# Kernel optimization log

Measured on AMD Instinct MI355X. Metric: run time of the kernel, lower is better.

Reference implementation:

```python
import jax, jax.numpy as jnp
import numpy as np

HID, H, KV, D = 2048, 16, 4, 128
B, L = 8, 1024
T = B * L
EPS = 1e-6
NEG = -1e9


def _rms(x, w):
    # RMSNorm over head_dim in fp32
    var = jnp.mean(x.astype(jnp.float32) ** 2, axis=-1, keepdims=True)
    return (x.astype(jnp.float32) * jax.lax.rsqrt(var + EPS)).astype(x.dtype) * w


def _rot_half(x):
    x1, x2 = jnp.split(x, 2, axis=-1)
    return jnp.concatenate([-x2, x1], axis=-1)


def setup_inputs() -> dict:
    key = jax.random.key(0)
    ks = jax.random.split(key, 24)
    inp = {}
    inp['packed_sequence'] = jax.random.normal(ks[0], (T, HID), jnp.float32) * 0.02
    # RoPE tables: positions restart per sample
    pos = jnp.tile(jnp.arange(L, dtype=jnp.float32), B)  # [T]
    inv_freq = 1.0 / (10000.0 ** (jnp.arange(0, D, 2, dtype=jnp.float32) / D))
    ang = pos[:, None] * inv_freq[None, :]  # [T, D/2]
    inp['cos'] = jnp.concatenate([jnp.cos(ang), jnp.cos(ang)], axis=-1)
    inp['sin'] = jnp.concatenate([jnp.sin(ang), jnp.sin(ang)], axis=-1)
    # per-sample causal additive mask [B, L, L]
    causal = jnp.tril(jnp.ones((L, L), bool))
    inp['attn_bias'] = jnp.broadcast_to(jnp.where(causal, 0.0, NEG).astype(jnp.float32), (B, L, L))
    inp['gen_mask'] = jax.random.randint(ks[1], (T,), 0, 2, jnp.int32)
    s = 0.02
    inp['Wq'] = jax.random.normal(ks[2], (H * D, HID), jnp.float32) * s
    inp['bq'] = jnp.zeros((H * D,), jnp.float32)
    inp['Wqg'] = jax.random.normal(ks[3], (H * D, HID), jnp.float32) * s
    inp['bqg'] = jnp.zeros((H * D,), jnp.float32)
    inp['Wk'] = jax.random.normal(ks[4], (KV * D, HID), jnp.float32) * s
    inp['bk'] = jnp.zeros((KV * D,), jnp.float32)
    inp['Wkg'] = jax.random.normal(ks[5], (KV * D, HID), jnp.float32) * s
    inp['bkg'] = jnp.zeros((KV * D,), jnp.float32)
    inp['Wv'] = jax.random.normal(ks[6], (KV * D, HID), jnp.float32) * s
    inp['bv'] = jnp.zeros((KV * D,), jnp.float32)
    inp['Wvg'] = jax.random.normal(ks[7], (KV * D, HID), jnp.float32) * s
    inp['bvg'] = jnp.zeros((KV * D,), jnp.float32)
    inp['Wo'] = jax.random.normal(ks[8], (HID, H * D), jnp.float32) * s
    inp['Wog'] = jax.random.normal(ks[9], (HID, H * D), jnp.float32) * s
    inp['q_norm_w'] = jnp.ones((D,), jnp.float32)
    inp['q_norm_gen_w'] = jnp.ones((D,), jnp.float32)
    inp['k_norm_w'] = jnp.ones((D,), jnp.float32)
    inp['k_norm_gen_w'] = jnp.ones((D,), jnp.float32)
    return inp


def reference(packed_sequence, cos, sin, attn_bias, gen_mask,
              Wq, bq, Wqg, bqg, Wk, bk, Wkg, bkg, Wv, bv, Wvg, bvg,
              Wo, Wog, q_norm_w, q_norm_gen_w, k_norm_w, k_norm_gen_w):
    route = (gen_mask > 0)[:, None]  # [T,1]; und/gen indexes partition tokens -> select
    # dual-path QKV projections (scatter into zero buffers == per-token select)
    q = jnp.where(route, packed_sequence @ Wqg.T + bqg, packed_sequence @ Wq.T + bq)
    k = jnp.where(route, packed_sequence @ Wkg.T + bkg, packed_sequence @ Wk.T + bk)
    v = jnp.where(route, packed_sequence @ Wvg.T + bvg, packed_sequence @ Wv.T + bv)
    q = q.reshape(T, H, D)
    k = k.reshape(T, KV, D)
    v = v.reshape(T, KV, D)
    rh = route[:, :, None]  # [T,1,1]
    # dual-path per-head-dim RMSNorm
    q = jnp.where(rh, _rms(q, q_norm_gen_w), _rms(q, q_norm_w))
    k = jnp.where(rh, _rms(k, k_norm_gen_w), _rms(k, k_norm_w))
    # RoPE (broadcast over heads, unsqueeze_dim=1)
    c, s = cos[:, None, :], sin[:, None, :]
    q = q * c + _rot_half(q) * s
    k = k * c + _rot_half(k) * s
    # GQA: repeat kv heads to H
    k = jnp.repeat(k, H // KV, axis=1)
    v = jnp.repeat(v, H // KV, axis=1)
    # ragged attention, equal sample lens -> batched SDPA with per-sample masks
    qb = q.reshape(B, L, H, D)
    kb = k.reshape(B, L, H, D)
    vb = v.reshape(B, L, H, D)
    scores = jnp.einsum('blhd,bmhd->bhlm', qb, kb) / np.sqrt(D).astype(np.float32)
    scores = scores + attn_bias[:, None, :, :]
    p = jax.nn.softmax(scores, axis=-1)
    o = jnp.einsum('bhlm,bmhd->blhd', p, vb).reshape(T, H * D)
    # dual-path output projection (no bias)
    return jnp.where(route, o @ Wog.T, o @ Wo.T)
```

## Files before the change

kernel.cpp:

```cpp
#include <hip/hip_runtime.h>

#define T_TOK 8192
#define HID   2048
#define NH    16
#define NKV   4
#define HD    128

typedef __attribute__((ext_vector_type(8))) short short8;
typedef __attribute__((ext_vector_type(4))) float f32x4;
typedef __attribute__((ext_vector_type(4))) unsigned short us4;

__device__ __forceinline__ unsigned short f2b(float f) {
  union { float f; unsigned int u; } x; x.f = f;
  unsigned int u = x.u;
  return (unsigned short)((u + 0x7FFFu + ((u >> 16) & 1u)) >> 16);
}
__device__ __forceinline__ float b2f(unsigned short u) {
  union { float f; unsigned int u; } x; x.u = ((unsigned int)u) << 16; return x.f;
}

__device__ __forceinline__ void ld_lds16(const unsigned short* g, unsigned short* l) {
  __builtin_amdgcn_global_load_lds(
      (const __attribute__((address_space(1))) unsigned int*)g,
      (__attribute__((address_space(3))) unsigned int*)l, 16, 0, 0);
}

__device__ __forceinline__ int xcd_swz(int orig, int nwg) {
  int q = nwg >> 3;
  return (orig & 7) * q + (orig >> 3);
}

__global__ __launch_bounds__(1024) void scan_route(const int* __restrict__ gm,
                                                   int* __restrict__ perm,
                                                   int* __restrict__ n0p) {
  __shared__ int cnt[1024];
  int tid = threadIdx.x;
  int base = tid * 8;
  int r[8]; int c0 = 0;
#pragma unroll
  for (int i = 0; i < 8; i++) { r[i] = gm[base + i] > 0 ? 1 : 0; c0 += 1 - r[i]; }
  cnt[tid] = c0;
  __syncthreads();
  for (int off = 1; off < 1024; off <<= 1) {
    int add = (tid >= off) ? cnt[tid - off] : 0;
    __syncthreads();
    cnt[tid] += add;
    __syncthreads();
  }
  int incl = cnt[tid];
  int total0 = cnt[1023];
  int p0 = incl - c0;
  int p1 = total0 + (base - (incl - c0));
#pragma unroll
  for (int i = 0; i < 8; i++) {
    int t = base + i;
    if (r[i] == 0) perm[p0++] = t;
    else           perm[p1++] = t;
  }
  if (tid == 0) n0p[0] = total0;
}

struct ConvArgs {
  const float* src[9];
  unsigned short* dst[9];
  int blk_end[9];
};

__global__ __launch_bounds__(256) void convert_all(ConvArgs a) {
  int blk = blockIdx.x;
  int s = 0;
  while (blk >= a.blk_end[s]) s++;
  int local = blk - (s ? a.blk_end[s - 1] : 0);
  int i = local * 1024 + threadIdx.x * 4;
  float4 v = *(const float4*)(a.src[s] + i);
  us4 o = { f2b(v.x), f2b(v.y), f2b(v.z), f2b(v.w) };
  *(us4*)(a.dst[s] + i) = o;
}

#define BM  128
#define BK  64

__device__ __forceinline__ void gemm_core(
    const unsigned short* __restrict__ Xb,
    const unsigned short* __restrict__ W,
    const float* __restrict__ bias,
    const int* __restrict__ perm,
    int r0, int r1, int col0, int N,
    float* __restrict__ outF, unsigned short* __restrict__ outB,
    unsigned short* As, unsigned short* Bs)
{
  int tid = threadIdx.x;
  int lane = tid & 63, wid = tid >> 6;
  int quad = lane >> 4, l15 = lane & 15;
  int wr = (wid >> 1) * 64, wc = (wid & 1) * 64;
  int lrow = lane >> 3;
  int sc8 = (lane & 7) ^ (lrow & 7);

  const unsigned short* ag[4]; const unsigned short* bg[4];
  unsigned short* al[4]; unsigned short* bl[4];
#pragma unroll
  for (int i = 0; i < 4; i++) {
    int row = wid * 32 + i * 8 + lrow;
    int gr = r0 + row; if (gr > r1 - 1) gr = r1 - 1;
    ag[i] = Xb + (size_t)perm[gr] * HID + sc8 * 8;
    bg[i] = W + (size_t)(col0 + row) * HID + sc8 * 8;
    al[i] = As + (wid * 32 + i * 8) * BK;
    bl[i] = Bs + (wid * 32 + i * 8) * BK;
  }

  f32x4 zero = {0.f, 0.f, 0.f, 0.f};
  f32x4 acc[4][4];
#pragma unroll
  for (int a = 0; a < 4; a++)
#pragma unroll
    for (int b = 0; b < 4; b++) acc[a][b] = zero;

  for (int k0 = 0; k0 < HID; k0 += BK) {
#pragma unroll
    for (int i = 0; i < 4; i++) {
      ld_lds16(ag[i] + k0, al[i]);
      ld_lds16(bg[i] + k0, bl[i]);
    }
    __syncthreads();
#pragma unroll
    for (int kk = 0; kk < 2; kk++) {
      int cswz = ((kk * 4 + quad) ^ (l15 & 7)) * 8;
      short8 af[4], bf[4];
#pragma unroll
      for (int mt = 0; mt < 4; mt++)
        af[mt] = *(const short8*)&As[(wr + mt * 16 + l15) * BK + cswz];
#pragma unroll
      for (int nt = 0; nt < 4; nt++)
        bf[nt] = *(const short8*)&Bs[(wc + nt * 16 + l15) * BK + cswz];
#pragma unroll
      for (int mt = 0; mt < 4; mt++)
#pragma unroll
        for (int nt = 0; nt < 4; nt++)
          acc[mt][nt] = __builtin_amdgcn_mfma_f32_16x16x32_bf16(af[mt], bf[nt], acc[mt][nt], 0, 0, 0);
    }
    __syncthreads();
  }

#pragma unroll
  for (int mt = 0; mt < 4; mt++) {
#pragma unroll
    for (int r = 0; r < 4; r++) {
      int lr = wr + mt * 16 + quad * 4 + r;
      int gr = r0 + lr;
      if (gr >= r1) continue;
      int tok = perm[gr];
#pragma unroll
      for (int nt = 0; nt < 4; nt++) {
        int col = col0 + wc + nt * 16 + l15;
        float v = acc[mt][nt][r];
        if (bias) v += bias[col];
        if (outF) outF[(size_t)tok * N + col] = v;
        else      outB[(size_t)tok * N + col] = f2b(v);
      }
    }
  }
}

#define QKV_GX 64
#define QKV_GY 24
__global__ __launch_bounds__(256, 3) void gemm_qkv(
    const unsigned short* __restrict__ xb,
    const unsigned short* wq0, const unsigned short* wq1,
    const float* bq0, const float* bq1,
    const unsigned short* wk0, const unsigned short* wk1,
    const float* bk0, const float* bk1,
    const unsigned short* wv0, const unsigned short* wv1,
    const float* bv0, const float* bv1,
    unsigned short* qraw, unsigned short* kraw, unsigned short* vb,
    const int* __restrict__ perm, const int* __restrict__ n0p)
{
  __shared__ unsigned short As[BM * BK];
  __shared__ unsigned short Bs[BM * BK];
  int orig = blockIdx.x + QKV_GX * (blockIdx.y + QKV_GY * blockIdx.z);
  int wg = xcd_swz(orig, QKV_GX * QKV_GY * 2);
  int bx = wg % QKV_GX, by = (wg / QKV_GX) % QKV_GY, set = wg / (QKV_GX * QKV_GY);

  int n0 = n0p[0];
  int r0, r1;
  if (set == 0) { r0 = bx * BM; if (r0 >= n0) return; r1 = (r0 + BM < n0) ? r0 + BM : n0; }
  else          { r0 = n0 + bx * BM; if (r0 >= T_TOK) return; r1 = (r0 + BM < T_TOK) ? r0 + BM : T_TOK; }
  const unsigned short* w; const float* bias;
  unsigned short* ob; int col0, N;
  if (by < 16)      { w = set ? wq1 : wq0; bias = set ? bq1 : bq0; col0 = by * 128;        N = HID; ob = qraw; }
  else if (by < 20) { w = set ? wk1 : wk0; bias = set ? bk1 : bk0; col0 = (by - 16) * 128; N = 512; ob = kraw; }
  else              { w = set ? wv1 : wv0; bias = set ? bv1 : bv0; col0 = (by - 20) * 128; N = 512; ob = vb; }
  gemm_core(xb, w, bias, perm, r0, r1, col0, N, nullptr, ob, As, Bs);
}

#define OUT_GX 64
#define OUT_GY 16
__global__ __launch_bounds__(256, 3) void gemm_out(
    const unsigned short* __restrict__ obuf,
    const unsigned short* wo0, const unsigned short* wo1,
    float* __restrict__ out,
    const int* __restrict__ perm, const int* __restrict__ n0p)
{
  __shared__ unsigned short As[BM * BK];
  __shared__ unsigned short Bs[BM * BK];
  int orig = blockIdx.x + OUT_GX * (blockIdx.y + OUT_GY * blockIdx.z);
  int wg = xcd_swz(orig, OUT_GX * OUT_GY * 2);
  int bx = wg % OUT_GX, by = (wg / OUT_GX) % OUT_GY, set = wg / (OUT_GX * OUT_GY);

  int n0 = n0p[0];
  int r0, r1;
  if (set == 0) { r0 = bx * BM; if (r0 >= n0) return; r1 = (r0 + BM < n0) ? r0 + BM : n0; }
  else          { r0 = n0 + bx * BM; if (r0 >= T_TOK) return; r1 = (r0 + BM < T_TOK) ? r0 + BM : T_TOK; }
  gemm_core(obuf, set ? wo1 : wo0, nullptr, perm, r0, r1, by * 128, HID, out, nullptr, As, Bs);
}

__global__ __launch_bounds__(256) void rms_rope_all(
    const unsigned short* __restrict__ qin, unsigned short* __restrict__ qout,
    const unsigned short* __restrict__ kin, unsigned short* __restrict__ kout,
    const float* __restrict__ cosb, const float* __restrict__ sinb,
    const int* __restrict__ gm,
    const float* __restrict__ qwn, const float* __restrict__ qwg,
    const float* __restrict__ kwn, const float* __restrict__ kwg)
{
  int wvid = blockIdx.x * 4 + (threadIdx.x >> 6);
  int lane = threadIdx.x & 63;
  const unsigned short* in; unsigned short* outp;
  const float* wn; const float* wg; int t, h, nh;
  if (wvid < T_TOK * NH) {
    in = qin; outp = qout; wn = qwn; wg = qwg; t = wvid >> 4; h = wvid & 15; nh = NH;
  } else {
    int w2 = wvid - T_TOK * NH;
    in = kin; outp = kout; wn = kwn; wg = kwg; t = w2 >> 2; h = w2 & 3; nh = NKV;
  }
  size_t off = ((size_t)t * nh + h) * HD;
  float x1 = b2f(in[off + lane]), x2 = b2f(in[off + 64 + lane]);
  float ss = x1 * x1 + x2 * x2;
#pragma unroll
  for (int o = 32; o > 0; o >>= 1) ss += __shfl_xor(ss, o, 64);
  float inv = rsqrtf(ss * (1.0f / 128.0f) + 1e-6f);
  const float* w = (gm[t] > 0) ? wg : wn;
  float n1 = x1 * inv * w[lane];
  float n2 = x2 * inv * w[lane + 64];
  float c1 = cosb[t * HD + lane],      s1 = sinb[t * HD + lane];
  float c2 = cosb[t * HD + 64 + lane], s2 = sinb[t * HD + 64 + lane];
  outp[off + lane]      = f2b(n1 * c1 - n2 * s1);
  outp[off + 64 + lane] = f2b(n2 * c2 + n1 * s2);
}

__global__ __launch_bounds__(256) void vtrans(const unsigned short* __restrict__ vb,
                                              unsigned short* __restrict__ vt) {
  __shared__ unsigned short Vs[64][136];
  int kt = blockIdx.x, kvh = blockIdx.y, b = blockIdx.z;
  int t = threadIdx.x;
  int kv0 = kt * 64;
  int key = t >> 2, c0 = t & 3;
#pragma unroll
  for (int i = 0; i < 4; i++) {
    int cc = c0 * 4 + i;
    *(short8*)&Vs[key][cc * 8] =
        *(const short8*)(vb + ((size_t)(b * 1024 + kv0 + key) * NKV + kvh) * HD + cc * 8);
  }
  __syncthreads();
  int d = t >> 1, hh = t & 1;
  unsigned short tmp[32];
#pragma unroll
  for (int k = 0; k < 32; k++) tmp[k] = Vs[hh * 32 + k][d];
  size_t base = ((size_t)(b * NKV + kvh) * HD + d) * 1024 + kv0 + hh * 32;
  *(short8*)(vt + base)      = *(short8*)&tmp[0];
  *(short8*)(vt + base + 8)  = *(short8*)&tmp[8];
  *(short8*)(vt + base + 16) = *(short8*)&tmp[16];
  *(short8*)(vt + base + 24) = *(short8*)&tmp[24];
}

__global__ __launch_bounds__(512, 4) void attn_kernel(
    const unsigned short* __restrict__ qb,
    const unsigned short* __restrict__ kb,
    const unsigned short* __restrict__ vt,
    unsigned short* __restrict__ ob)
{
  __shared__ unsigned short Ks[2][64 * 128];
  __shared__ unsigned short Vt[2][128 * 64];
  __shared__ unsigned short Ps[8 * 16 * 64];
  int orig = blockIdx.x + 16 * (blockIdx.y + 4 * blockIdx.z);
  int wg = xcd_swz(orig, 16 * 4 * 8);
  int pslot = wg % 16, kvh = (wg / 16) % 4, b = wg / 64;

  int tid = threadIdx.x, lane = tid & 63, wid = tid >> 6;
  int quad = lane >> 4, l15 = lane & 15;
  int h = kvh * 4 + (wid >> 1);
  int g = wid & 1;
  const float sc = 0.088388347648318447f;
  f32x4 zero = {0.f, 0.f, 0.f, 0.f};

  int skey = (wid << 2) + (lane >> 4);
  int kswz = ((lane & 15) ^ (skey & 7)) * 8;
  int sd   = (wid << 3) + (lane >> 3);
  int vswz = ((lane & 7) ^ (sd & 7)) * 8;

  auto stageKV = [&](int buf, int kv0) {
#pragma unroll
    for (int i = 0; i < 2; i++) {
      int key = i * 32 + skey;
      ld_lds16(kb + ((size_t)(b * 1024 + kv0 + key) * NKV + kvh) * HD + kswz,
               &Ks[buf][(size_t)(i * 32 + (wid << 2)) * 128]);
    }
#pragma unroll
    for (int i = 0; i < 2; i++) {
      int d = i * 64 + sd;
      ld_lds16(vt + ((size_t)(b * NKV + kvh) * HD + d) * 1024 + kv0 + vswz,
               &Vt[buf][(size_t)(i * 64 + (wid << 3)) * 64]);
    }
  };

  for (int half = 0; half < 2; half++) {
    int a = half ? (31 - pslot) : pslot;
    int q0 = a * 32;
    int qrow = q0 + g * 16 + l15;
    size_t qoff = ((size_t)(b * 1024 + qrow) * NH + h) * HD;
    short8 qfr[4];
#pragma unroll
    for (int kk = 0; kk < 4; kk++)
      qfr[kk] = *(const short8*)(qb + qoff + kk * 32 + quad * 8);

    f32x4 oacc[8];
#pragma unroll
    for (int i = 0; i < 8; i++) oacc[i] = zero;
    float lpart[4] = {0.f, 0.f, 0.f, 0.f};

    int ktiles = a / 2 + 1;
    stageKV(0, 0);
    int cur = 0;

    for (int kt = 0; kt < ktiles; kt++) {
      int kv0 = kt * 64;
      bool hasnext = (kt + 1 < ktiles);
      if (hasnext) {
        stageKV(cur ^ 1, kv0 + 64);
        asm volatile("s_waitcnt vmcnt(4)" ::: "memory");
      } else {
        asm volatile("s_waitcnt vmcnt(0)" ::: "memory");
      }
      __builtin_amdgcn_s_barrier();
      __builtin_amdgcn_sched_barrier(0);
      const unsigned short* ksb = Ks[cur];
      const unsigned short* vvb = Vt[cur];
      bool lastt = (kt == ktiles - 1);

      f32x4 s[4];
      __builtin_amdgcn_s_setprio(1);
#pragma unroll
      for (int g4 = 0; g4 < 4; g4++) {
        f32x4 acc = zero;
#pragma unroll
        for (int kk = 0; kk < 4; kk++) {
          short8 bfr = *(const short8*)&ksb[(g4 * 16 + l15) * 128 + ((kk * 4 + quad) ^ (l15 & 7)) * 8];
          acc = __builtin_amdgcn_mfma_f32_16x16x32_bf16(qfr[kk], bfr, acc, 0, 0, 0);
        }
        s[g4] = acc;
      }
      __builtin_amdgcn_s_setprio(0);

      int rowb = q0 + g * 16 + quad * 4;
#pragma unroll
      for (int g4 = 0; g4 < 4; g4++) {
        int col = kv0 + g4 * 16 + l15;
        int k8 = g4 * 2 + (l15 >> 3);
#pragma unroll
        for (int r = 0; r < 4; r++) {
          float p = __expf(s[g4][r] * sc);
          if (lastt && col > rowb + r) p = 0.f;
          lpart[r] += p;
          int row = quad * 4 + r;
          Ps[wid * 1024 + row * 64 + ((k8 ^ (row & 7)) * 8 + (l15 & 7))] = f2b(p);
        }
      }

      __builtin_amdgcn_s_setprio(1);
#pragma unroll
      for (int kk = 0; kk < 2; kk++) {
        short8 pa = *(const short8*)&Ps[wid * 1024 + l15 * 64 + ((kk * 4 + quad) ^ (l15 & 7)) * 8];
#pragma unroll
        for (int dg = 0; dg < 8; dg++) {
          short8 vf = *(const short8*)&vvb[(dg * 16 + l15) * 64 + ((kk * 4 + quad) ^ (l15 & 7)) * 8];
          oacc[dg] = __builtin_amdgcn_mfma_f32_16x16x32_bf16(pa, vf, oacc[dg], 0, 0, 0);
        }
      }
      __builtin_amdgcn_s_setprio(0);

      __builtin_amdgcn_s_barrier();
      __builtin_amdgcn_sched_barrier(0);
      cur ^= 1;
    }

#pragma unroll
    for (int r = 0; r < 4; r++) {
      float v = lpart[r];
#pragma unroll
      for (int o = 8; o > 0; o >>= 1) v += __shfl_xor(v, o, 64);
      lpart[r] = 1.0f / v;
    }
#pragma unroll
    for (int dg = 0; dg < 8; dg++)
#pragma unroll
      for (int r = 0; r < 4; r++) {
        int row = q0 + g * 16 + quad * 4 + r;
        ob[((size_t)(b * 1024 + row) * NH + h) * HD + dg * 16 + l15] =
            f2b(oacc[dg][r] * lpart[r]);
      }
  }
}

extern "C" void kernel_launch(void* const* d_in, const int* in_sizes, int n_in,
                              void* d_out, int out_size, void* d_ws, size_t ws_size,
                              hipStream_t stream) {
  const float* x    = (const float*)d_in[0];
  const float* cosb = (const float*)d_in[1];
  const float* sinb = (const float*)d_in[2];
  const int*   gm   = (const int*)d_in[4];
  const float* Wq   = (const float*)d_in[5];
  const float* bq   = (const float*)d_in[6];
  const float* Wqg  = (const float*)d_in[7];
  const float* bqg  = (const float*)d_in[8];
  const float* Wk   = (const float*)d_in[9];
  const float* bk   = (const float*)d_in[10];
  const float* Wkg  = (const float*)d_in[11];
  const float* bkg  = (const float*)d_in[12];
  const float* Wv   = (const float*)d_in[13];
  const float* bv   = (const float*)d_in[14];
  const float* Wvg  = (const float*)d_in[15];
  const float* bvg  = (const float*)d_in[16];
  const float* Wo   = (const float*)d_in[17];
  const float* Wog  = (const float*)d_in[18];
  const float* qnw  = (const float*)d_in[19];
  const float* qngw = (const float*)d_in[20];
  const float* knw  = (const float*)d_in[21];
  const float* kngw = (const float*)d_in[22];
  float* out = (float*)d_out;

  char* wsb = (char*)d_ws;
  size_t off = 0;
  auto alloc = [&](size_t bytes) -> char* {
    char* p = wsb + off;
    off += (bytes + 255) & ~(size_t)255;
    return p;
  };
  int* perm = (int*)alloc((size_t)T_TOK * 4);
  int* n0p  = (int*)alloc(4);
  unsigned short* xb  = (unsigned short*)alloc((size_t)T_TOK * HID * 2);
  unsigned short* wq0 = (unsigned short*)alloc((size_t)HID * HID * 2);
  unsigned short* wq1 = (unsigned short*)alloc((size_t)HID * HID * 2);
  unsigned short* wk0 = (unsigned short*)alloc((size_t)512 * HID * 2);
  unsigned short* wk1 = (unsigned short*)alloc((size_t)512 * HID * 2);
  unsigned short* wv0 = (unsigned short*)alloc((size_t)512 * HID * 2);
  unsigned short* wv1 = (unsigned short*)alloc((size_t)512 * HID * 2);
  unsigned short* wo0 = (unsigned short*)alloc((size_t)HID * HID * 2);
  unsigned short* wo1 = (unsigned short*)alloc((size_t)HID * HID * 2);
  unsigned short* qraw = (unsigned short*)alloc((size_t)T_TOK * HID * 2);
  unsigned short* kraw = (unsigned short*)alloc((size_t)T_TOK * 512 * 2);
  unsigned short* vbuf = (unsigned short*)alloc((size_t)T_TOK * 512 * 2);
  unsigned short* vtb  = (unsigned short*)alloc((size_t)T_TOK * 512 * 2);
  unsigned short* qbuf = (unsigned short*)alloc((size_t)T_TOK * HID * 2);
  unsigned short* kbuf = (unsigned short*)alloc((size_t)T_TOK * 512 * 2);
  unsigned short* obuf = qraw;

  scan_route<<<dim3(1), dim3(1024), 0, stream>>>(gm, perm, n0p);

  ConvArgs ca;
  const float* srcs[9] = {x, Wq, Wqg, Wk, Wkg, Wv, Wvg, Wo, Wog};
  unsigned short* dsts[9] = {xb, wq0, wq1, wk0, wk1, wv0, wv1, wo0, wo1};
  int ns[9] = {T_TOK * HID, HID * HID, HID * HID, 512 * HID, 512 * HID,
               512 * HID, 512 * HID, HID * HID, HID * HID};
  int cum = 0;
  for (int i = 0; i < 9; i++) {
    ca.src[i] = srcs[i]; ca.dst[i] = dsts[i];
    cum += ns[i] / 1024; ca.blk_end[i] = cum;
  }
  convert_all<<<dim3(cum), dim3(256), 0, stream>>>(ca);

  gemm_qkv<<<dim3(QKV_GX, QKV_GY, 2), dim3(256), 0, stream>>>(
      xb, wq0, wq1, bq, bqg, wk0, wk1, bk, bkg, wv0, wv1, bv, bvg,
      qraw, kraw, vbuf, perm, n0p);

  rms_rope_all<<<dim3(T_TOK * (NH + NKV) / 4), dim3(256), 0, stream>>>(
      qraw, qbuf, kraw, kbuf, cosb, sinb, gm, qnw, qngw, knw, kngw);
  vtrans<<<dim3(16, 4, 8), dim3(256), 0, stream>>>(vbuf, vtb);

  attn_kernel<<<dim3(16, 4, 8), dim3(512), 0, stream>>>(qbuf, kbuf, vtb, obuf);

  gemm_out<<<dim3(OUT_GX, OUT_GY, 2), dim3(256), 0, stream>>>(obuf, wo0, wo1, out, perm, n0p);
}
```

Baseline: 572.0 us.

## Fold route scan and V transpose into neighbouring kernels, remap GEMM tile order

The route scan now runs as one extra block of the conversion kernel, and the V transpose runs as extra blocks of the RMSNorm/RoPE kernel, which removes two kernel launches and the serial single-block scan launch. The QKV and output GEMMs replace the XCD swizzle with a custom mapping that places paired row tiles, and every column tile of both weight sets, on the same XCD so A tiles are reused in that XCD's L2. The scan block shares the conversion launch, so it may finish late, and the fused kernel now reserves LDS in every block, including RoPE blocks that never use it.

```diff
diff --git a/kernel.cpp b/kernel.cpp
--- a/kernel.cpp
+++ b/kernel.cpp
@@ -30,44 +30,65 @@
   return (orig & 7) * q + (orig >> 3);
 }
 
-__global__ __launch_bounds__(1024) void scan_route(const int* __restrict__ gm,
-                                                   int* __restrict__ perm,
-                                                   int* __restrict__ n0p) {
-  __shared__ int cnt[1024];
-  int tid = threadIdx.x;
-  int base = tid * 8;
-  int r[8]; int c0 = 0;
-#pragma unroll
-  for (int i = 0; i < 8; i++) { r[i] = gm[base + i] > 0 ? 1 : 0; c0 += 1 - r[i]; }
-  cnt[tid] = c0;
-  __syncthreads();
-  for (int off = 1; off < 1024; off <<= 1) {
-    int add = (tid >= off) ? cnt[tid - off] : 0;
-    __syncthreads();
-    cnt[tid] += add;
-    __syncthreads();
-  }
-  int incl = cnt[tid];
-  int total0 = cnt[1023];
-  int p0 = incl - c0;
-  int p1 = total0 + (base - (incl - c0));
-#pragma unroll
-  for (int i = 0; i < 8; i++) {
-    int t = base + i;
-    if (r[i] == 0) perm[p0++] = t;
-    else           perm[p1++] = t;
-  }
-  if (tid == 0) n0p[0] = total0;
+__device__ __forceinline__ void qkv_map(int orig, int& bx, int& by, int& set) {
+  int xcd = orig & 7;
+  int wl = orig >> 3;
+  int g = wl / 96;
+  int rem = wl - g * 96;
+  int p = rem >> 1;
+  int e = rem & 1;
+  bx = (g * 2 + e) * 8 + xcd;
+  set = p / 24; by = p - set * 24;
+}
+__device__ __forceinline__ void out_map(int orig, int& bx, int& by, int& set) {
+  int xcd = orig & 7;
+  int wl = orig >> 3;
+  int g = wl / 64;
+  int rem = wl - g * 64;
+  int p = rem >> 1;
+  int e = rem & 1;
+  bx = (g * 2 + e) * 8 + xcd;
+  set = p / 16; by = p - set * 16;
 }
 
 struct ConvArgs {
   const float* src[9];
   unsigned short* dst[9];
   int blk_end[9];
+  const int* gm; int* perm; int* n0p;
 };
 
 __global__ __launch_bounds__(256) void convert_all(ConvArgs a) {
   int blk = blockIdx.x;
+  int nconv = a.blk_end[8];
+  if (blk == nconv) {
+    __shared__ int cnt[256];
+    int t = threadIdx.x;
+    int base = t * 32;
+    int c = 0;
+#pragma unroll
+    for (int i = 0; i < 32; i++) c += (a.gm[base + i] > 0) ? 0 : 1;
+    cnt[t] = c;
+    __syncthreads();
+    for (int off = 1; off < 256; off <<= 1) {
+      int add = (t >= off) ? cnt[t - off] : 0;
+      __syncthreads();
+      cnt[t] += add;
+      __syncthreads();
+    }
+    int incl = cnt[t];
+    int total0 = cnt[255];
+    int p0 = incl - c;
+    int p1 = total0 + base - p0;
+#pragma unroll
+    for (int i = 0; i < 32; i++) {
+      int tok = base + i;
+      if (a.gm[tok] > 0) a.perm[p1++] = tok;
+      else               a.perm[p0++] = tok;
+    }
+    if (t == 0) a.n0p[0] = total0;
+    return;
+  }
   int s = 0;
   while (blk >= a.blk_end[s]) s++;
   int local = blk - (s ? a.blk_end[s - 1] : 0);
@@ -177,8 +198,8 @@
   __shared__ unsigned short As[BM * BK];
   __shared__ unsigned short Bs[BM * BK];
   int orig = blockIdx.x + QKV_GX * (blockIdx.y + QKV_GY * blockIdx.z);
-  int wg = xcd_swz(orig, QKV_GX * QKV_GY * 2);
-  int bx = wg % QKV_GX, by = (wg / QKV_GX) % QKV_GY, set = wg / (QKV_GX * QKV_GY);
+  int bx, by, set;
+  qkv_map(orig, bx, by, set);
 
   int n0 = n0p[0];
   int r0, r1;
@@ -203,8 +224,8 @@
   __shared__ unsigned short As[BM * BK];
   __shared__ unsigned short Bs[BM * BK];
   int orig = blockIdx.x + OUT_GX * (blockIdx.y + OUT_GY * blockIdx.z);
-  int wg = xcd_swz(orig, OUT_GX * OUT_GY * 2);
-  int bx = wg % OUT_GX, by = (wg / OUT_GX) % OUT_GY, set = wg / (OUT_GX * OUT_GY);
+  int bx, by, set;
+  out_map(orig, bx, by, set);
 
   int n0 = n0p[0];
   int r0, r1;
@@ -213,14 +234,42 @@
   gemm_core(obuf, set ? wo1 : wo0, nullptr, perm, r0, r1, by * 128, HID, out, nullptr, As, Bs);
 }
 
-__global__ __launch_bounds__(256) void rms_rope_all(
+#define RR_BLOCKS (T_TOK * (NH + NKV) / 4)
+
+__global__ __launch_bounds__(256) void rope_vtrans(
     const unsigned short* __restrict__ qin, unsigned short* __restrict__ qout,
     const unsigned short* __restrict__ kin, unsigned short* __restrict__ kout,
     const float* __restrict__ cosb, const float* __restrict__ sinb,
     const int* __restrict__ gm,
     const float* __restrict__ qwn, const float* __restrict__ qwg,
-    const float* __restrict__ kwn, const float* __restrict__ kwg)
+    const float* __restrict__ kwn, const float* __restrict__ kwg,
+    const unsigned short* __restrict__ vb, unsigned short* __restrict__ vt)
 {
+  __shared__ unsigned short Vs[64][136];
+  if (blockIdx.x >= RR_BLOCKS) {
+    int idx = blockIdx.x - RR_BLOCKS;
+    int kt = idx & 15, kvh = (idx >> 4) & 3, b = idx >> 6;
+    int t = threadIdx.x;
+    int kv0 = kt * 64;
+    int key = t >> 2, c0 = t & 3;
+#pragma unroll
+    for (int i = 0; i < 4; i++) {
+      int cc = c0 * 4 + i;
+      *(short8*)&Vs[key][cc * 8] =
+          *(const short8*)(vb + ((size_t)(b * 1024 + kv0 + key) * NKV + kvh) * HD + cc * 8);
+    }
+    __syncthreads();
+    int d = t >> 1, hh = t & 1;
+    unsigned short tmp[32];
+#pragma unroll
+    for (int k = 0; k < 32; k++) tmp[k] = Vs[hh * 32 + k][d];
+    size_t base = ((size_t)(b * NKV + kvh) * HD + d) * 1024 + kv0 + hh * 32;
+    *(short8*)(vt + base)      = *(short8*)&tmp[0];
+    *(short8*)(vt + base + 8)  = *(short8*)&tmp[8];
+    *(short8*)(vt + base + 16) = *(short8*)&tmp[16];
+    *(short8*)(vt + base + 24) = *(short8*)&tmp[24];
+    return;
+  }
   int wvid = blockIdx.x * 4 + (threadIdx.x >> 6);
   int lane = threadIdx.x & 63;
   const unsigned short* in; unsigned short* outp;
@@ -244,31 +293,6 @@
   float c2 = cosb[t * HD + 64 + lane], s2 = sinb[t * HD + 64 + lane];
   outp[off + lane]      = f2b(n1 * c1 - n2 * s1);
   outp[off + 64 + lane] = f2b(n2 * c2 + n1 * s2);
-}
-
-__global__ __launch_bounds__(256) void vtrans(const unsigned short* __restrict__ vb,
-                                              unsigned short* __restrict__ vt) {
-  __shared__ unsigned short Vs[64][136];
-  int kt = blockIdx.x, kvh = blockIdx.y, b = blockIdx.z;
-  int t = threadIdx.x;
-  int kv0 = kt * 64;
-  int key = t >> 2, c0 = t & 3;
-#pragma unroll
-  for (int i = 0; i < 4; i++) {
-    int cc = c0 * 4 + i;
-    *(short8*)&Vs[key][cc * 8] =
-        *(const short8*)(vb + ((size_t)(b * 1024 + kv0 + key) * NKV + kvh) * HD + cc * 8);
-  }
-  __syncthreads();
-  int d = t >> 1, hh = t & 1;
-  unsigned short tmp[32];
-#pragma unroll
-  for (int k = 0; k < 32; k++) tmp[k] = Vs[hh * 32 + k][d];
-  size_t base = ((size_t)(b * NKV + kvh) * HD + d) * 1024 + kv0 + hh * 32;
-  *(short8*)(vt + base)      = *(short8*)&tmp[0];
-  *(short8*)(vt + base + 8)  = *(short8*)&tmp[8];
-  *(short8*)(vt + base + 16) = *(short8*)&tmp[16];
-  *(short8*)(vt + base + 24) = *(short8*)&tmp[24];
 }
 
 __global__ __launch_bounds__(512, 4) void attn_kernel(
@@ -462,8 +486,6 @@
   unsigned short* kbuf = (unsigned short*)alloc((size_t)T_TOK * 512 * 2);
   unsigned short* obuf = qraw;
 
-  scan_route<<<dim3(1), dim3(1024), 0, stream>>>(gm, perm, n0p);
-
   ConvArgs ca;
   const float* srcs[9] = {x, Wq, Wqg, Wk, Wkg, Wv, Wvg, Wo, Wog};
   unsigned short* dsts[9] = {xb, wq0, wq1, wk0, wk1, wv0, wv1, wo0, wo1};
@@ -474,15 +496,15 @@
     ca.src[i] = srcs[i]; ca.dst[i] = dsts[i];
     cum += ns[i] / 1024; ca.blk_end[i] = cum;
   }
-  convert_all<<<dim3(cum), dim3(256), 0, stream>>>(ca);
+  ca.gm = gm; ca.perm = perm; ca.n0p = n0p;
+  convert_all<<<dim3(cum + 1), dim3(256), 0, stream>>>(ca);
 
   gemm_qkv<<<dim3(QKV_GX, QKV_GY, 2), dim3(256), 0, stream>>>(
       xb, wq0, wq1, bq, bqg, wk0, wk1, bk, bkg, wv0, wv1, bv, bvg,
       qraw, kraw, vbuf, perm, n0p);
 
-  rms_rope_all<<<dim3(T_TOK * (NH + NKV) / 4), dim3(256), 0, stream>>>(
-      qraw, qbuf, kraw, kbuf, cosb, sinb, gm, qnw, qngw, knw, kngw);
-  vtrans<<<dim3(16, 4, 8), dim3(256), 0, stream>>>(vbuf, vtb);
+  rope_vtrans<<<dim3(RR_BLOCKS + 512), dim3(256), 0, stream>>>(
+      qraw, qbuf, kraw, kbuf, cosb, sinb, gm, qnw, qngw, knw, kngw, vbuf, vtb);
 
   attn_kernel<<<dim3(16, 4, 8), dim3(512), 0, stream>>>(qbuf, kbuf, vtb, obuf);
 
```

Result: faster. 555.9 us (-2.8%).
